# Kernel tuning notes

Measured on AMD Instinct MI355X. Metric: run time of the kernel, lower is better.

The kernel has to match this reference:

```python
import jax, jax.numpy as jnp
import numpy as np

MARGIN = 0.25
SCALE = 64.0
OP = 1.0 + MARGIN
ON = -MARGIN
DELTA_P = 1.0 - MARGIN
DELTA_N = MARGIN
NEG_FILL = -1e4  # effectively -inf for these logits (|logit| < ~300)

B, D = 8192, 1024
N_IDS = 512


def setup_inputs() -> dict:
    key = jax.random.key(0)
    k1, k2 = jax.random.split(key)
    inputs = jax.random.normal(k1, (B, D), dtype=jnp.float32)
    targets = jax.random.randint(k2, (B,), 0, N_IDS, dtype=jnp.int64)
    return {"inputs": inputs, "targets": targets}


def reference(inputs, targets):
    # L2-normalize embeddings (torch F.normalize uses eps=1e-12 clamp on norm)
    norm = jnp.maximum(jnp.linalg.norm(inputs, axis=1, keepdims=True), 1e-12)
    x = inputs / norm
    sim = x @ x.T  # [B, B] cosine similarities

    same = targets[:, None] == targets[None, :]
    eye = jnp.eye(targets.shape[0], dtype=bool)
    pos_mask = same & ~eye
    neg_mask = ~same

    sim_sg = jax.lax.stop_gradient(sim)  # .detach() in original
    ap = jnp.maximum(OP - sim_sg, 0.0)
    an = jnp.maximum(sim_sg - ON, 0.0)

    logit_p = -ap * (sim - DELTA_P) * SCALE
    logit_n = an * (sim - DELTA_N) * SCALE

    lse_p = jax.nn.logsumexp(jnp.where(pos_mask, logit_p, NEG_FILL), axis=1)
    lse_n = jax.nn.logsumexp(jnp.where(neg_mask, logit_n, NEG_FILL), axis=1)

    loss_i = jax.nn.softplus(lse_n + lse_p)  # [B]
    valid = pos_mask.any(axis=1) & neg_mask.any(axis=1)

    total = jnp.sum(jnp.where(valid, loss_i, 0.0))
    count = jnp.maximum(jnp.sum(valid), 1)
    return total / count
```

## Files before the change

### kernel.cpp

```cpp
#include <hip/hip_runtime.h>
#include <hip/hip_bf16.h>
#include <math.h>

#define THREADS 256
typedef unsigned short ushortT;
typedef __attribute__((ext_vector_type(8))) short bf16x8;
typedef __attribute__((ext_vector_type(4))) float f32x4;

__device__ __forceinline__ void async16(const ushortT* g, ushortT* l) {
  __builtin_amdgcn_global_load_lds(
      (const __attribute__((address_space(1))) unsigned int*)g,
      (__attribute__((address_space(3))) unsigned int*)l, 16, 0, 0);
}

__device__ __forceinline__ ushortT f2bf(float f) {
  __hip_bfloat16 h = __float2bfloat16(f);
  return *reinterpret_cast<ushortT*>(&h);
}

__global__ __launch_bounds__(THREADS) void k_prep(const float* __restrict__ x,
                                                  ushortT* __restrict__ xn, int D) {
  __shared__ float red[4];
  const int row = blockIdx.x;
  const int tid = threadIdx.x;
  const int gid = row * (D / 4) + tid;
  const float4 v = reinterpret_cast<const float4*>(x)[gid];
  float s = v.x * v.x + v.y * v.y + v.z * v.z + v.w * v.w;
  #pragma unroll
  for (int off = 32; off; off >>= 1) s += __shfl_xor(s, off);
  if ((tid & 63) == 0) red[tid >> 6] = s;
  __syncthreads();
  const float tot = red[0] + red[1] + red[2] + red[3];
  const float rn = 1.0f / fmaxf(sqrtf(tot), 1e-12f);
  ushort4 o;
  o.x = f2bf(v.x * rn); o.y = f2bf(v.y * rn);
  o.z = f2bf(v.z * rn); o.w = f2bf(v.w * rn);
  reinterpret_cast<ushort4*>(xn)[gid] = o;
}

__global__ __launch_bounds__(THREADS, 4) void k_main_mfma(const ushortT* __restrict__ xn,
                                                          const int* __restrict__ tgt,
                                                          float4* __restrict__ partial,
                                                          int D, int nb) {
  __shared__ ushortT Asm[128 * 32];
  __shared__ ushortT Bsm[128 * 32];

  const int tid = threadIdx.x;
  const int lane = tid & 63;
  const int w = tid >> 6;

  const int b = blockIdx.x;
  int bi = (int)((2.f * nb + 1.f -
                  sqrtf((2.f * nb + 1.f) * (2.f * nb + 1.f) - 8.f * (float)b)) * 0.5f);
  while ((bi + 1) * (2 * nb - bi) / 2 <= b) ++bi;
  while (bi * (2 * nb - bi + 1) / 2 > b) --bi;
  const int bj = bi + (b - bi * (2 * nb - bi + 1) / 2);
  const bool isdiag = (bi == bj);

  const int i0 = bi * 128, j0 = bj * 128;
  const int wr = (w >> 1) * 64, wc = (w & 1) * 64;

  const int sr = lane & 15, sc = lane >> 4;
  const ushortT* baseA = xn + (size_t)i0 * D;
  const ushortT* baseB = xn + (size_t)j0 * D;
  const int offA = (w * 16 + sr) * D + sc * 8;
  const int hstep = 64 * D;
  ushortT* lA0 = &Asm[w * 512];
  ushortT* lA1 = &Asm[(w + 4) * 512];
  ushortT* lB0 = &Bsm[w * 512];
  ushortT* lB1 = &Bsm[(w + 4) * 512];

  const ushortT* Bbase = isdiag ? Asm : Bsm;
  const int aoff = ((w >> 1) * 4) * 512 + lane * 8;
  const int boff = ((w & 1) * 4) * 512 + lane * 8;

  f32x4 acc[4][4];
  #pragma unroll
  for (int mt = 0; mt < 4; ++mt)
    #pragma unroll
    for (int nt = 0; nt < 4; ++nt)
      acc[mt][nt] = (f32x4){0.f, 0.f, 0.f, 0.f};

  const int kiters = D / 32;
  for (int kk = 0; kk < kiters; ++kk) {
    const int ko = kk * 32;
    async16(baseA + offA + ko, lA0);
    async16(baseA + offA + hstep + ko, lA1);
    if (!isdiag) {
      async16(baseB + offA + ko, lB0);
      async16(baseB + offA + hstep + ko, lB1);
    }
    __syncthreads();
    bf16x8 afr[4];
    #pragma unroll
    for (int mt = 0; mt < 4; ++mt)
      afr[mt] = *reinterpret_cast<const bf16x8*>(&Asm[aoff + mt * 512]);
    {
      bf16x8 b0 = *reinterpret_cast<const bf16x8*>(&Bbase[boff]);
      bf16x8 b1 = *reinterpret_cast<const bf16x8*>(&Bbase[boff + 512]);
      #pragma unroll
      for (int mt = 0; mt < 4; ++mt)
        acc[mt][0] = __builtin_amdgcn_mfma_f32_16x16x32_bf16(afr[mt], b0, acc[mt][0], 0, 0, 0);
      #pragma unroll
      for (int mt = 0; mt < 4; ++mt)
        acc[mt][1] = __builtin_amdgcn_mfma_f32_16x16x32_bf16(afr[mt], b1, acc[mt][1], 0, 0, 0);
      b0 = *reinterpret_cast<const bf16x8*>(&Bbase[boff + 2 * 512]);
      b1 = *reinterpret_cast<const bf16x8*>(&Bbase[boff + 3 * 512]);
      #pragma unroll
      for (int mt = 0; mt < 4; ++mt)
        acc[mt][2] = __builtin_amdgcn_mfma_f32_16x16x32_bf16(afr[mt], b0, acc[mt][2], 0, 0, 0);
      #pragma unroll
      for (int mt = 0; mt < 4; ++mt)
        acc[mt][3] = __builtin_amdgcn_mfma_f32_16x16x32_bf16(afr[mt], b1, acc[mt][3], 0, 0, 0);
    }
    __syncthreads();
  }

  const int q = lane >> 4, c = lane & 15;
  int tj[4];
  #pragma unroll
  for (int nt = 0; nt < 4; ++nt) tj[nt] = tgt[j0 + wc + nt * 16 + c];
  int tir[16];
  #pragma unroll
  for (int mt = 0; mt < 4; ++mt) {
    const int4 t4 = *reinterpret_cast<const int4*>(tgt + i0 + wr + mt * 16 + q * 4);
    tir[mt * 4 + 0] = t4.x; tir[mt * 4 + 1] = t4.y;
    tir[mt * 4 + 2] = t4.z; tir[mt * 4 + 3] = t4.w;
  }

  #pragma unroll
  for (int mt = 0; mt < 4; ++mt) {
    #pragma unroll
    for (int reg = 0; reg < 4; ++reg) {
      const int i = i0 + wr + mt * 16 + q * 4 + reg;
      const int ti = tir[mt * 4 + reg];
      float m = -1e30f, sn = 0.f;
      float sel[4];
      #pragma unroll
      for (int nt = 0; nt < 4; ++nt) {
        const float s = acc[mt][nt][reg];
        const int j = j0 + wc + nt * 16 + c;
        const bool same = (tj[nt] == ti);
        const bool vpos = same && (j != i);
        const float lp = (fminf(s, 1.25f) - 1.25f) * fmaf(s, 64.f, -48.f);
        const float sv = vpos ? lp : -2e30f;
        sel[nt] = sv;
        m = fmaxf(m, sv);
        const float ln = (fmaxf(s, -0.25f) + 0.25f) * fmaf(s, 64.f, -16.f);
        const float en = __expf(ln);
        sn += same ? 0.f : en;
      }
      #pragma unroll
      for (int off = 1; off < 16; off <<= 1) m = fmaxf(m, __shfl_xor(m, off));
      float sp = 0.f;
      #pragma unroll
      for (int nt = 0; nt < 4; ++nt) sp += __expf(sel[nt] - m);
      #pragma unroll
      for (int off = 1; off < 16; off <<= 1) {
        sp += __shfl_xor(sp, off);
        sn += __shfl_xor(sn, off);
      }
      if (c == 0) {
        float4 o; o.x = m; o.y = sp; o.z = 0.f; o.w = sn;
        partial[((size_t)i * nb + bj) * 2 + (w & 1)] = o;
      }
    }
  }

  if (!isdiag) {
    #pragma unroll
    for (int nt = 0; nt < 4; ++nt) {
      const int jt = tj[nt];
      const int jrow = j0 + wc + nt * 16 + c;
      float m = -1e30f, sn = 0.f;
      #pragma unroll
      for (int mt = 0; mt < 4; ++mt) {
        #pragma unroll
        for (int reg = 0; reg < 4; ++reg) {
          const float s = acc[mt][nt][reg];
          const bool same = (tir[mt * 4 + reg] == jt);
          const float lp = (fminf(s, 1.25f) - 1.25f) * fmaf(s, 64.f, -48.f);
          m = fmaxf(m, same ? lp : -2e30f);
          const float ln = (fmaxf(s, -0.25f) + 0.25f) * fmaf(s, 64.f, -16.f);
          const float en = __expf(ln);
          sn += same ? 0.f : en;
        }
      }
      m = fmaxf(m, __shfl_xor(m, 16));
      m = fmaxf(m, __shfl_xor(m, 32));
      float sp = 0.f;
      #pragma unroll
      for (int mt = 0; mt < 4; ++mt) {
        #pragma unroll
        for (int reg = 0; reg < 4; ++reg) {
          const float s = acc[mt][nt][reg];
          const bool same = (tir[mt * 4 + reg] == jt);
          const float lp = (fminf(s, 1.25f) - 1.25f) * fmaf(s, 64.f, -48.f);
          sp += __expf((same ? lp : -2e30f) - m);
        }
      }
      sp += __shfl_xor(sp, 16); sp += __shfl_xor(sp, 32);
      sn += __shfl_xor(sn, 16); sn += __shfl_xor(sn, 32);
      if (lane < 16) {
        float4 o; o.x = m; o.y = sp; o.z = 0.f; o.w = sn;
        partial[((size_t)jrow * nb + bi) * 2 + (w >> 1)] = o;
      }
    }
  }
}

__global__ __launch_bounds__(THREADS) void k_reduce(const float4* __restrict__ partial,
                                                    float* __restrict__ row_loss) {
  const int lane = threadIdx.x & 63;
  const int row = blockIdx.x * 4 + (threadIdx.x >> 6);
  const float4 a = partial[(size_t)row * 128 + lane];
  const float4 b = partial[(size_t)row * 128 + 64 + lane];
  float mp = fmaxf(a.x, b.x);
  float sp = a.y * __expf(a.x - mp) + b.y * __expf(b.x - mp);
  float sn = a.w + b.w;
  #pragma unroll
  for (int off = 1; off < 64; off <<= 1) {
    const float m2 = __shfl_xor(mp, off), s2 = __shfl_xor(sp, off);
    const float nm = fmaxf(mp, m2);
    sp = sp * __expf(mp - nm) + s2 * __expf(m2 - nm);
    mp = nm;
    sn += __shfl_xor(sn, off);
  }
  if (lane == 0) {
    float loss = -1.0f;
    if (sp > 0.f && sn > 0.f) {
      const float z = mp + logf(sp) + logf(sn);
      loss = (z > 0.f) ? (z + log1pf(__expf(-z))) : log1pf(__expf(z));
    }
    row_loss[row] = loss;
  }
}

__global__ __launch_bounds__(THREADS) void k_final(const float* __restrict__ row_loss,
                                                   float* __restrict__ out, int B) {
  __shared__ float ssum[4];
  __shared__ float scnt[4];
  const int tid = threadIdx.x;
  float sum = 0.f, cnt = 0.f;
  for (int i = tid; i < B; i += THREADS) {
    const float l = row_loss[i];
    if (l >= 0.f) { sum += l; cnt += 1.f; }
  }
  #pragma unroll
  for (int off = 32; off; off >>= 1) {
    sum += __shfl_xor(sum, off);
    cnt += __shfl_xor(cnt, off);
  }
  if ((tid & 63) == 0) { ssum[tid >> 6] = sum; scnt[tid >> 6] = cnt; }
  __syncthreads();
  if (tid == 0) {
    float ts = 0.f, tc = 0.f;
    #pragma unroll
    for (int w = 0; w < 4; ++w) { ts += ssum[w]; tc += scnt[w]; }
    out[0] = ts / fmaxf(tc, 1.f);
  }
}

extern "C" void kernel_launch(void* const* d_in, const int* in_sizes, int n_in,
                              void* d_out, int out_size, void* d_ws, size_t ws_size,
                              hipStream_t stream) {
  const float* x = (const float*)d_in[0];
  const int* tgt = (const int*)d_in[1];
  float* out = (float*)d_out;
  const int B = in_sizes[1];
  const int D = in_sizes[0] / B;
  const int nb = B / 128;

  ushortT* xn = (ushortT*)d_ws;
  float4* partial = (float4*)((char*)d_ws + (size_t)B * D * 2);
  float* row_loss = (float*)((char*)d_ws + (size_t)B * D * 2 + (size_t)B * 2 * nb * 16);

  k_prep<<<B, THREADS, 0, stream>>>(x, xn, D);
  k_main_mfma<<<nb * (nb + 1) / 2, THREADS, 0, stream>>>(xn, tgt, partial, D, nb);
  k_reduce<<<B / 4, THREADS, 0, stream>>>(partial, row_loss);
  k_final<<<1, THREADS, 0, stream>>>(row_loss, out, B);
}
```

Measured before the change: 261.5 us.

## Double-buffer LDS tiles to prefetch the next K-slice during MFMA compute

The shared-memory A and B tiles become two buffers each. Async global-to-LDS loads for the next K-slice are issued before the MFMAs on the current slice run, which leaves one barrier per iteration instead of two. The aim is to hide global-load latency behind matrix-core work. In exchange, LDS use per block doubles and the launch-bounds occupancy hint drops from 4 to 2 blocks, which may lower occupancy.

```diff
diff --git a/kernel.cpp b/kernel.cpp
--- a/kernel.cpp
+++ b/kernel.cpp
@@ -38,12 +38,12 @@
   reinterpret_cast<ushort4*>(xn)[gid] = o;
 }
 
-__global__ __launch_bounds__(THREADS, 4) void k_main_mfma(const ushortT* __restrict__ xn,
+__global__ __launch_bounds__(THREADS, 2) void k_main_mfma(const ushortT* __restrict__ xn,
                                                           const int* __restrict__ tgt,
                                                           float4* __restrict__ partial,
                                                           int D, int nb) {
-  __shared__ ushortT Asm[128 * 32];
-  __shared__ ushortT Bsm[128 * 32];
+  __shared__ ushortT Asm[2][128 * 32];
+  __shared__ ushortT Bsm[2][128 * 32];
 
   const int tid = threadIdx.x;
   const int lane = tid & 63;
@@ -65,12 +65,7 @@
   const ushortT* baseB = xn + (size_t)j0 * D;
   const int offA = (w * 16 + sr) * D + sc * 8;
   const int hstep = 64 * D;
-  ushortT* lA0 = &Asm[w * 512];
-  ushortT* lA1 = &Asm[(w + 4) * 512];
-  ushortT* lB0 = &Bsm[w * 512];
-  ushortT* lB1 = &Bsm[(w + 4) * 512];
-
-  const ushortT* Bbase = isdiag ? Asm : Bsm;
+
   const int aoff = ((w >> 1) * 4) * 512 + lane * 8;
   const int boff = ((w & 1) * 4) * 512 + lane * 8;
 
@@ -82,38 +77,56 @@
       acc[mt][nt] = (f32x4){0.f, 0.f, 0.f, 0.f};
 
   const int kiters = D / 32;
+
+  {
+    async16(baseA + offA, &Asm[0][w * 512]);
+    async16(baseA + offA + hstep, &Asm[0][(w + 4) * 512]);
+    if (!isdiag) {
+      async16(baseB + offA, &Bsm[0][w * 512]);
+      async16(baseB + offA + hstep, &Bsm[0][(w + 4) * 512]);
+    }
+  }
+  __syncthreads();
+
+  int cur = 0;
   for (int kk = 0; kk < kiters; ++kk) {
-    const int ko = kk * 32;
-    async16(baseA + offA + ko, lA0);
-    async16(baseA + offA + hstep + ko, lA1);
-    if (!isdiag) {
-      async16(baseB + offA + ko, lB0);
-      async16(baseB + offA + hstep + ko, lB1);
+    if (kk + 1 < kiters) {
+      const int ko = (kk + 1) * 32;
+      const int nxt = cur ^ 1;
+      async16(baseA + offA + ko, &Asm[nxt][w * 512]);
+      async16(baseA + offA + hstep + ko, &Asm[nxt][(w + 4) * 512]);
+      if (!isdiag) {
+        async16(baseB + offA + ko, &Bsm[nxt][w * 512]);
+        async16(baseB + offA + hstep + ko, &Bsm[nxt][(w + 4) * 512]);
+      }
+    }
+
+    const ushortT* Ab = Asm[cur];
+    const ushortT* Bb = isdiag ? Asm[cur] : Bsm[cur];
+    bf16x8 afr[4];
+    #pragma unroll
+    for (int mt = 0; mt < 4; ++mt)
+      afr[mt] = *reinterpret_cast<const bf16x8*>(&Ab[aoff + mt * 512]);
+    {
+      bf16x8 b0 = *reinterpret_cast<const bf16x8*>(&Bb[boff]);
+      bf16x8 b1 = *reinterpret_cast<const bf16x8*>(&Bb[boff + 512]);
+      #pragma unroll
+      for (int mt = 0; mt < 4; ++mt)
+        acc[mt][0] = __builtin_amdgcn_mfma_f32_16x16x32_bf16(afr[mt], b0, acc[mt][0], 0, 0, 0);
+      #pragma unroll
+      for (int mt = 0; mt < 4; ++mt)
+        acc[mt][1] = __builtin_amdgcn_mfma_f32_16x16x32_bf16(afr[mt], b1, acc[mt][1], 0, 0, 0);
+      b0 = *reinterpret_cast<const bf16x8*>(&Bb[boff + 2 * 512]);
+      b1 = *reinterpret_cast<const bf16x8*>(&Bb[boff + 3 * 512]);
+      #pragma unroll
+      for (int mt = 0; mt < 4; ++mt)
+        acc[mt][2] = __builtin_amdgcn_mfma_f32_16x16x32_bf16(afr[mt], b0, acc[mt][2], 0, 0, 0);
+      #pragma unroll
+      for (int mt = 0; mt < 4; ++mt)
+        acc[mt][3] = __builtin_amdgcn_mfma_f32_16x16x32_bf16(afr[mt], b1, acc[mt][3], 0, 0, 0);
     }
     __syncthreads();
-    bf16x8 afr[4];
-    #pragma unroll
-    for (int mt = 0; mt < 4; ++mt)
-      afr[mt] = *reinterpret_cast<const bf16x8*>(&Asm[aoff + mt * 512]);
-    {
-      bf16x8 b0 = *reinterpret_cast<const bf16x8*>(&Bbase[boff]);
-      bf16x8 b1 = *reinterpret_cast<const bf16x8*>(&Bbase[boff + 512]);
-      #pragma unroll
-      for (int mt = 0; mt < 4; ++mt)
-        acc[mt][0] = __builtin_amdgcn_mfma_f32_16x16x32_bf16(afr[mt], b0, acc[mt][0], 0, 0, 0);
-      #pragma unroll
-      for (int mt = 0; mt < 4; ++mt)
-        acc[mt][1] = __builtin_amdgcn_mfma_f32_16x16x32_bf16(afr[mt], b1, acc[mt][1], 0, 0, 0);
-      b0 = *reinterpret_cast<const bf16x8*>(&Bbase[boff + 2 * 512]);
-      b1 = *reinterpret_cast<const bf16x8*>(&Bbase[boff + 3 * 512]);
-      #pragma unroll
-      for (int mt = 0; mt < 4; ++mt)
-        acc[mt][2] = __builtin_amdgcn_mfma_f32_16x16x32_bf16(afr[mt], b0, acc[mt][2], 0, 0, 0);
-      #pragma unroll
-      for (int mt = 0; mt < 4; ++mt)
-        acc[mt][3] = __builtin_amdgcn_mfma_f32_16x16x32_bf16(afr[mt], b1, acc[mt][3], 0, 0, 0);
-    }
-    __syncthreads();
+    cur ^= 1;
   }
 
   const int q = lane >> 4, c = lane & 15;
```

Result: faster. 251.8 us (-3.7%).

## Load MFMA fragments directly from global memory with register double-buffering

Applied to the files above, without the earlier changes.

Drops the LDS staging of A/B tiles and the per-iteration barriers. Each wave now loads its bf16 MFMA fragments straight from global memory into registers, double-buffered across two k-steps so loads overlap with MFMA work. Occupancy hint is lowered from 4 to 3 to make room for the extra registers. The catch is that tiles are no longer shared across waves through LDS, so global and L2 traffic goes up: each row fragment is fetched by two waves. The diagonal-tile reuse of A as B is also lost.

```diff
diff --git a/kernel.cpp b/kernel.cpp
--- a/kernel.cpp
+++ b/kernel.cpp
@@ -6,12 +6,6 @@
 typedef unsigned short ushortT;
 typedef __attribute__((ext_vector_type(8))) short bf16x8;
 typedef __attribute__((ext_vector_type(4))) float f32x4;
-
-__device__ __forceinline__ void async16(const ushortT* g, ushortT* l) {
-  __builtin_amdgcn_global_load_lds(
-      (const __attribute__((address_space(1))) unsigned int*)g,
-      (__attribute__((address_space(3))) unsigned int*)l, 16, 0, 0);
-}
 
 __device__ __forceinline__ ushortT f2bf(float f) {
   __hip_bfloat16 h = __float2bfloat16(f);
@@ -38,13 +32,10 @@
   reinterpret_cast<ushort4*>(xn)[gid] = o;
 }
 
-__global__ __launch_bounds__(THREADS, 4) void k_main_mfma(const ushortT* __restrict__ xn,
+__global__ __launch_bounds__(THREADS, 3) void k_main_mfma(const ushortT* __restrict__ xn,
                                                           const int* __restrict__ tgt,
                                                           float4* __restrict__ partial,
                                                           int D, int nb) {
-  __shared__ ushortT Asm[128 * 32];
-  __shared__ ushortT Bsm[128 * 32];
-
   const int tid = threadIdx.x;
   const int lane = tid & 63;
   const int w = tid >> 6;
@@ -60,19 +51,15 @@
   const int i0 = bi * 128, j0 = bj * 128;
   const int wr = (w >> 1) * 64, wc = (w & 1) * 64;
 
-  const int sr = lane & 15, sc = lane >> 4;
-  const ushortT* baseA = xn + (size_t)i0 * D;
-  const ushortT* baseB = xn + (size_t)j0 * D;
-  const int offA = (w * 16 + sr) * D + sc * 8;
-  const int hstep = 64 * D;
-  ushortT* lA0 = &Asm[w * 512];
-  ushortT* lA1 = &Asm[(w + 4) * 512];
-  ushortT* lB0 = &Bsm[w * 512];
-  ushortT* lB1 = &Bsm[(w + 4) * 512];
-
-  const ushortT* Bbase = isdiag ? Asm : Bsm;
-  const int aoff = ((w >> 1) * 4) * 512 + lane * 8;
-  const int boff = ((w & 1) * 4) * 512 + lane * 8;
+  const int fr = lane & 15, fc = lane >> 4;
+  const ushortT* gA[4];
+  const ushortT* gB[4];
+  #pragma unroll
+  for (int mt = 0; mt < 4; ++mt)
+    gA[mt] = xn + (size_t)(i0 + wr + mt * 16 + fr) * D + fc * 8;
+  #pragma unroll
+  for (int nt = 0; nt < 4; ++nt)
+    gB[nt] = xn + (size_t)(j0 + wc + nt * 16 + fr) * D + fc * 8;
 
   f32x4 acc[4][4];
   #pragma unroll
@@ -82,38 +69,41 @@
       acc[mt][nt] = (f32x4){0.f, 0.f, 0.f, 0.f};
 
   const int kiters = D / 32;
-  for (int kk = 0; kk < kiters; ++kk) {
-    const int ko = kk * 32;
-    async16(baseA + offA + ko, lA0);
-    async16(baseA + offA + hstep + ko, lA1);
-    if (!isdiag) {
-      async16(baseB + offA + ko, lB0);
-      async16(baseB + offA + hstep + ko, lB1);
-    }
-    __syncthreads();
-    bf16x8 afr[4];
+
+  bf16x8 a0[4], b0[4], a1[4], b1[4];
+  #pragma unroll
+  for (int t = 0; t < 4; ++t) {
+    a0[t] = *reinterpret_cast<const bf16x8*>(gA[t]);
+    b0[t] = *reinterpret_cast<const bf16x8*>(gB[t]);
+  }
+
+  for (int kk = 0; kk < kiters; kk += 2) {
+    {
+      const int ko = (kk + 1) * 32;
+      #pragma unroll
+      for (int t = 0; t < 4; ++t) {
+        a1[t] = *reinterpret_cast<const bf16x8*>(gA[t] + ko);
+        b1[t] = *reinterpret_cast<const bf16x8*>(gB[t] + ko);
+      }
+    }
     #pragma unroll
     for (int mt = 0; mt < 4; ++mt)
-      afr[mt] = *reinterpret_cast<const bf16x8*>(&Asm[aoff + mt * 512]);
-    {
-      bf16x8 b0 = *reinterpret_cast<const bf16x8*>(&Bbase[boff]);
-      bf16x8 b1 = *reinterpret_cast<const bf16x8*>(&Bbase[boff + 512]);
-      #pragma unroll
-      for (int mt = 0; mt < 4; ++mt)
-        acc[mt][0] = __builtin_amdgcn_mfma_f32_16x16x32_bf16(afr[mt], b0, acc[mt][0], 0, 0, 0);
-      #pragma unroll
-      for (int mt = 0; mt < 4; ++mt)
-        acc[mt][1] = __builtin_amdgcn_mfma_f32_16x16x32_bf16(afr[mt], b1, acc[mt][1], 0, 0, 0);
-      b0 = *reinterpret_cast<const bf16x8*>(&Bbase[boff + 2 * 512]);
-      b1 = *reinterpret_cast<const bf16x8*>(&Bbase[boff + 3 * 512]);
-      #pragma unroll
-      for (int mt = 0; mt < 4; ++mt)
-        acc[mt][2] = __builtin_amdgcn_mfma_f32_16x16x32_bf16(afr[mt], b0, acc[mt][2], 0, 0, 0);
-      #pragma unroll
-      for (int mt = 0; mt < 4; ++mt)
-        acc[mt][3] = __builtin_amdgcn_mfma_f32_16x16x32_bf16(afr[mt], b1, acc[mt][3], 0, 0, 0);
-    }
-    __syncthreads();
+      #pragma unroll
+      for (int nt = 0; nt < 4; ++nt)
+        acc[mt][nt] = __builtin_amdgcn_mfma_f32_16x16x32_bf16(a0[mt], b0[nt], acc[mt][nt], 0, 0, 0);
+    if (kk + 2 < kiters) {
+      const int ko = (kk + 2) * 32;
+      #pragma unroll
+      for (int t = 0; t < 4; ++t) {
+        a0[t] = *reinterpret_cast<const bf16x8*>(gA[t] + ko);
+        b0[t] = *reinterpret_cast<const bf16x8*>(gB[t] + ko);
+      }
+    }
+    #pragma unroll
+    for (int mt = 0; mt < 4; ++mt)
+      #pragma unroll
+      for (int nt = 0; nt < 4; ++nt)
+        acc[mt][nt] = __builtin_amdgcn_mfma_f32_16x16x32_bf16(a1[mt], b1[nt], acc[mt][nt], 0, 0, 0);
   }
 
   const int q = lane >> 4, c = lane & 15;
```

Result: slower. 356.2 us (+36.2%).
